# Kernel tuning notes

Hardware: AMD Instinct MI355X
Metric: run time of the kernel (lower is better)

The kernel has to match this reference:

```python
import jax, jax.numpy as jnp
import numpy as np

D_MODEL = 1024
N_HEADS = 16
D_K = D_MODEL // N_HEADS
D_FF = 4096
LN_EPS = 1e-5


def _layer_norm(x, gamma, beta):
    mu = jnp.mean(x, axis=-1, keepdims=True)
    var = jnp.mean(jnp.square(x - mu), axis=-1, keepdims=True)
    return (x - mu) * jax.lax.rsqrt(var + LN_EPS) * gamma + beta


def setup_inputs() -> dict:
    key = jax.random.key(0)
    ks = jax.random.split(key, 16)
    B, S = 2, 2048
    x = jax.random.normal(ks[0], (B, S, D_MODEL), dtype=jnp.float32)
    # causal mask: True = masked (as used by masked_fill)
    mask = ~jnp.tril(jnp.ones((S, S), dtype=bool))
    s = 1.0 / np.sqrt(D_MODEL)
    sf = 1.0 / np.sqrt(D_FF)
    inp = {
        "x": x,
        "mask": mask,
        "ln1_g": jnp.ones((D_MODEL,), jnp.float32),
        "ln1_b": jnp.zeros((D_MODEL,), jnp.float32),
        "ln2_g": jnp.ones((D_MODEL,), jnp.float32),
        "ln2_b": jnp.zeros((D_MODEL,), jnp.float32),
        "Wq": jax.random.normal(ks[1], (D_MODEL, D_MODEL), jnp.float32) * s,
        "bq": jax.random.normal(ks[2], (D_MODEL,), jnp.float32) * s,
        "Wk": jax.random.normal(ks[3], (D_MODEL, D_MODEL), jnp.float32) * s,
        "bk": jax.random.normal(ks[4], (D_MODEL,), jnp.float32) * s,
        "Wv": jax.random.normal(ks[5], (D_MODEL, D_MODEL), jnp.float32) * s,
        "bv": jax.random.normal(ks[6], (D_MODEL,), jnp.float32) * s,
        "Wo": jax.random.normal(ks[7], (D_MODEL, D_MODEL), jnp.float32) * s,
        "bo": jax.random.normal(ks[8], (D_MODEL,), jnp.float32) * s,
        "W1": jax.random.normal(ks[9], (D_MODEL, D_FF), jnp.float32) * s,
        "b1": jax.random.normal(ks[10], (D_FF,), jnp.float32) * s,
        "W2": jax.random.normal(ks[11], (D_FF, D_MODEL), jnp.float32) * sf,
        "b2": jax.random.normal(ks[12], (D_MODEL,), jnp.float32) * sf,
    }
    return inp


def reference(x, mask, ln1_g, ln1_b, ln2_g, ln2_b,
              Wq, bq, Wk, bk, Wv, bv, Wo, bo, W1, b1, W2, b2):
    B, S, _ = x.shape
    normed = _layer_norm(x, ln1_g, ln1_b)
    # project and split heads: [B, H, S, Dk]
    def split_heads(t):
        return t.reshape(B, S, N_HEADS, D_K).transpose(0, 2, 1, 3)
    Q = split_heads(normed @ Wq + bq)
    K = split_heads(normed @ Wk + bk)
    V = split_heads(normed @ Wv + bv)
    qk = jnp.einsum("bhsd,bhtd->bhst", Q, K)  # [B, H, S, S]
    qk = jnp.where(mask, -jnp.inf, qk)  # mask applied BEFORE scaling, as in source
    attn = jax.nn.softmax(qk / np.sqrt(D_K), axis=-1)
    attn_out = jnp.einsum("bhst,bhtd->bhsd", attn, V)
    attn_out = attn_out.transpose(0, 2, 1, 3).reshape(B, S, D_MODEL)
    attn_out = attn_out @ Wo + bo
    res = attn_out + x  # dropout_p=0 (eval)
    h = _layer_norm(res, ln2_g, ln2_b)
    h = jax.nn.gelu(h @ W1 + b1, approximate=False)
    h = h @ W2 + b2
    return res + h
```

## Files before the change

### kernel.cpp

```cpp
#include <hip/hip_runtime.h>


typedef __bf16 bf16;
typedef __bf16 bf16x8 __attribute__((ext_vector_type(8)));
typedef float f32x4 __attribute__((ext_vector_type(4)));

#define NROWS 4096
#define DM 1024
#define SEQ 2048
#define NHEAD 16
#define DKH 64
#define DFF 4096
#define QSCALE 0.18033688f

#define GLL16(gptr, lptr) \
  __builtin_amdgcn_global_load_lds((const __attribute__((address_space(1))) void*)(gptr), \
                                   (__attribute__((address_space(3))) void*)(lptr), 16, 0, 0)

static char* g_scratch = nullptr;
namespace {
struct ScratchInit {
  ScratchInit() {
    void* p = nullptr;
    if (hipMalloc(&p, (size_t)128 * 1024 * 1024) == hipSuccess) g_scratch = (char*)p;
  }
};
static ScratchInit g_scratch_init;
}

__global__ __launch_bounds__(256) void ln_kernel(const float* __restrict__ inp,
                                                 const float* __restrict__ gamma,
                                                 const float* __restrict__ beta,
                                                 bf16* __restrict__ out) {
  int row = blockIdx.x;
  int t = threadIdx.x;
  float4 xv = *((const float4*)(inp + (size_t)row * DM) + t);
  float v[4] = {xv.x, xv.y, xv.z, xv.w};
  float s = 0.f, sq = 0.f;
#pragma unroll
  for (int i = 0; i < 4; i++) { s += v[i]; sq += v[i] * v[i]; }
#pragma unroll
  for (int m = 32; m >= 1; m >>= 1) { s += __shfl_xor(s, m); sq += __shfl_xor(sq, m); }
  __shared__ float rs[4], rq[4];
  int w = t >> 6, lane = t & 63;
  if (lane == 0) { rs[w] = s; rq[w] = sq; }
  __syncthreads();
  s = rs[0] + rs[1] + rs[2] + rs[3];
  sq = rq[0] + rq[1] + rq[2] + rq[3];
  float mu = s * (1.f / DM);
  float var = sq * (1.f / DM) - mu * mu;
  float rinv = rsqrtf(var + 1e-5f);
  float4 gv = *((const float4*)gamma + t);
  float4 bv = *((const float4*)beta + t);
  float g[4] = {gv.x, gv.y, gv.z, gv.w}, b[4] = {bv.x, bv.y, bv.z, bv.w};
  bf16 ov[4];
#pragma unroll
  for (int i = 0; i < 4; i++) ov[i] = (bf16)((v[i] - mu) * rinv * g[i] + b[i]);
  *(uint2*)(out + (size_t)row * DM + t * 4) = *(uint2*)ov;
}

__global__ __launch_bounds__(256) void concat_bias(const float* __restrict__ bq,
                                                   const float* __restrict__ bk,
                                                   const float* __restrict__ bv,
                                                   float* __restrict__ cat) {
  int i = blockIdx.x * 256 + threadIdx.x;
  float v = (i < 1024) ? bq[i] : (i < 2048 ? bk[i - 1024] : bv[i - 2048]);
  cat[i] = v;
}

__global__ __launch_bounds__(1024) void transpose_f32_bf16(const float* __restrict__ in,
                                                           bf16* __restrict__ out,
                                                           int R, int C) {
  __shared__ bf16 tile[32][33];
  int x = blockIdx.x * 32 + threadIdx.x;
  int y = blockIdx.y * 32 + threadIdx.y;
  tile[threadIdx.y][threadIdx.x] = (bf16)in[(size_t)y * C + x];
  __syncthreads();
  int ox = blockIdx.y * 32 + threadIdx.x;
  int oy = blockIdx.x * 32 + threadIdx.y;
  out[(size_t)oy * R + ox] = tile[threadIdx.x][threadIdx.y];
}

__global__ __launch_bounds__(1024) void transpose_bf16(const bf16* __restrict__ in,
                                                       bf16* __restrict__ out,
                                                       int R, int C) {
  __shared__ bf16 tile[32][33];
  size_t zoff = (size_t)blockIdx.z * (size_t)R * (size_t)C;
  int x = blockIdx.x * 32 + threadIdx.x;
  int y = blockIdx.y * 32 + threadIdx.y;
  tile[threadIdx.y][threadIdx.x] = in[zoff + (size_t)y * C + x];
  __syncthreads();
  int ox = blockIdx.y * 32 + threadIdx.x;
  int oy = blockIdx.x * 32 + threadIdx.y;
  out[zoff + (size_t)oy * R + ox] = tile[threadIdx.x][threadIdx.y];
}

#define BM 128
#define BK 64

#define EPI_QKV3 0
#define EPI_ATTN_RES 1
#define EPI_GELU 2
#define EPI_FFN2 3

template<int EPI, int BNT>
__global__ __launch_bounds__(256, 2) void gemm_bt(
    const bf16* __restrict__ A, const bf16* __restrict__ Bt,
    const float* __restrict__ bias, int Kd, int N,
    bf16* __restrict__ outb, float* __restrict__ outf,
    const float* __restrict__ add) {
  constexpr int MS = (BNT == 128) ? 4 : 2;
  __shared__ bf16 As[BM * BK];
  __shared__ bf16 Bs[BNT * BK];
  int t = threadIdx.x;
  int m0 = blockIdx.y * BM, n0 = blockIdx.x * BNT;
  int w = t >> 6, lane = t & 63, ln = lane & 15, quad = lane >> 4;
  int wm = (BNT == 128) ? (w >> 1) * 64 : w * 32;
  int wn = (BNT == 128) ? (w & 1) * 64 : 0;
  f32x4 acc[MS][4];
#pragma unroll
  for (int i = 0; i < MS; i++)
#pragma unroll
    for (int j = 0; j < 4; j++) acc[i][j] = (f32x4){0.f, 0.f, 0.f, 0.f};

  int lr = (t >> 3) & 7, lc = t & 7;
  int gcol = ((lc ^ lr) * 8);
  const bf16* Ab = A + (size_t)(m0 + w * 8 + lr) * Kd + gcol;
  const bf16* Bb = Bt + (size_t)(n0 + w * 8 + lr) * Kd + gcol;
  bf16* AsW = As + (w * 8) * BK;
  bf16* BsW = Bs + (w * 8) * BK;

  for (int k0 = 0; k0 < Kd; k0 += BK) {
    __syncthreads();
#pragma unroll
    for (int j = 0; j < 4; j++)
      GLL16(Ab + (size_t)(32 * j) * Kd + k0, AsW + 32 * j * BK);
#pragma unroll
    for (int j = 0; j < BNT / 32; j++)
      GLL16(Bb + (size_t)(32 * j) * Kd + k0, BsW + 32 * j * BK);
    __syncthreads();
#pragma unroll
    for (int kk = 0; kk < 2; kk++) {
      bf16x8 af[MS], bfr[4];
#pragma unroll
      for (int ms = 0; ms < MS; ms++) {
        int r = wm + ms * 16 + ln;
        af[ms] = *(const bf16x8*)(As + r * BK + (((kk * 4 + quad) ^ (r & 7)) * 8));
      }
#pragma unroll
      for (int ns = 0; ns < 4; ns++) {
        int r = wn + ns * 16 + ln;
        bfr[ns] = *(const bf16x8*)(Bs + r * BK + (((kk * 4 + quad) ^ (r & 7)) * 8));
      }
#pragma unroll
      for (int ms = 0; ms < MS; ms++)
#pragma unroll
        for (int ns = 0; ns < 4; ns++)
          acc[ms][ns] = __builtin_amdgcn_mfma_f32_16x16x32_bf16(af[ms], bfr[ns], acc[ms][ns], 0, 0, 0);
    }
  }

#pragma unroll
  for (int ms = 0; ms < MS; ms++) {
#pragma unroll
    for (int ns = 0; ns < 4; ns++) {
      int col = n0 + wn + ns * 16 + ln;
      float bv = bias[col];
#pragma unroll
      for (int r = 0; r < 4; r++) {
        int row = m0 + wm + ms * 16 + quad * 4 + r;
        float val = acc[ms][ns][r] + bv;
        if (EPI == EPI_QKV3) {
          int which = col >> 10, cc = col & 1023;
          int h = cc >> 6, dk = cc & 63;
          float sc = (which == 0) ? QSCALE : 1.f;
          int b = row >> 11, sx = row & 2047;
          outb[(size_t)which * (4 << 20) +
               ((((size_t)b * NHEAD + h) * SEQ) + sx) * DKH + dk] = (bf16)(val * sc);
        } else if (EPI == EPI_ATTN_RES) {
          size_t idx = (size_t)row * DM + col;
          outf[idx] = val + add[idx];
        } else if (EPI == EPI_GELU) {
          float gl = 0.5f * val * (1.f + erff(val * 0.7071067811865475f));
          outb[(size_t)row * N + col] = (bf16)gl;
        } else {
          size_t idx = (size_t)row * DM + col;
          outf[idx] = val + add[idx];
        }
      }
    }
  }
}

#define LSTR 72
#define OSTR 68

__global__ __launch_bounds__(256) void attn_kernel(
    const bf16* __restrict__ Q, const bf16* __restrict__ K,
    const bf16* __restrict__ Vt, bf16* __restrict__ out) {
  __shared__ float smem[4608];
  int lin = blockIdx.x;
  int bh = lin & 31;
  int ii = lin >> 5;
  int t = threadIdx.x, w = t >> 6, lane = t & 63, ln = lane & 15, quad = lane >> 4;
  size_t bhS = (size_t)bh * SEQ;
  const bf16* Vg0 = Vt + (size_t)bh * DKH * SEQ;
  bf16* Pw = (bf16*)smem + w * 32 * LSTR;

  bf16x8 ones;
#pragma unroll
  for (int i = 0; i < 8; i++) ones[i] = (bf16)1.0f;

  for (int half = 0; half < 2; half++) {
    int qq = half ? ii : (63 - ii);
    int qbase = qq * 32;

    bf16x8 qa[2][2];
#pragma unroll
    for (int m = 0; m < 2; m++)
#pragma unroll
      for (int ks = 0; ks < 2; ks++)
        qa[m][ks] = *(const bf16x8*)(Q + (bhS + qbase + m * 16 + ln) * DKH + ks * 32 + quad * 8);

    f32x4 o[2][4];
#pragma unroll
    for (int m = 0; m < 2; m++)
#pragma unroll
      for (int i = 0; i < 4; i++) o[m][i] = (f32x4){0.f, 0.f, 0.f, 0.f};
    f32x4 accl[2] = {(f32x4){0.f, 0.f, 0.f, 0.f}, (f32x4){0.f, 0.f, 0.f, 0.f}};

    int ktmax = qq >> 1;
    for (int kt = w; kt <= ktmax; kt += 4) {
      const bf16* Kg = K + (bhS + kt * 64) * DKH;
      bf16x8 kbf[8], vbf[8];
#pragma unroll
      for (int ns = 0; ns < 4; ns++)
#pragma unroll
        for (int ks = 0; ks < 2; ks++)
          kbf[ns * 2 + ks] = *(const bf16x8*)(Kg + (ns * 16 + ln) * DKH + ks * 32 + quad * 8);
#pragma unroll
      for (int ns = 0; ns < 4; ns++)
#pragma unroll
        for (int ks = 0; ks < 2; ks++)
          vbf[ns * 2 + ks] = *(const bf16x8*)(Vg0 + (size_t)(ns * 16 + ln) * SEQ + kt * 64 + ks * 32 + quad * 8);

      f32x4 s[2][4];
#pragma unroll
      for (int m = 0; m < 2; m++)
#pragma unroll
        for (int ns = 0; ns < 4; ns++) s[m][ns] = (f32x4){0.f, 0.f, 0.f, 0.f};
#pragma unroll
      for (int ns = 0; ns < 4; ns++)
#pragma unroll
        for (int m = 0; m < 2; m++) {
          s[m][ns] = __builtin_amdgcn_mfma_f32_16x16x32_bf16(qa[m][0], kbf[ns * 2], s[m][ns], 0, 0, 0);
          s[m][ns] = __builtin_amdgcn_mfma_f32_16x16x32_bf16(qa[m][1], kbf[ns * 2 + 1], s[m][ns], 0, 0, 0);
        }
      if (kt == ktmax) {
#pragma unroll
        for (int m = 0; m < 2; m++)
#pragma unroll
          for (int ns = 0; ns < 4; ns++)
#pragma unroll
            for (int r = 0; r < 4; r++) {
              int qrow = qbase + m * 16 + quad * 4 + r;
              int kpos = kt * 64 + ns * 16 + ln;
              if (kpos > qrow) s[m][ns][r] = -30000.f;
            }
      }
#pragma unroll
      for (int m = 0; m < 2; m++)
#pragma unroll
        for (int ns = 0; ns < 4; ns++)
#pragma unroll
          for (int r = 0; r < 4; r++)
            Pw[(m * 16 + quad * 4 + r) * LSTR + ns * 16 + ln] =
                (bf16)__builtin_amdgcn_exp2f(s[m][ns][r]);
      bf16x8 pa[2][2];
#pragma unroll
      for (int m = 0; m < 2; m++) {
        pa[m][0] = *(const bf16x8*)(Pw + (m * 16 + ln) * LSTR + quad * 8);
        pa[m][1] = *(const bf16x8*)(Pw + (m * 16 + ln) * LSTR + 32 + quad * 8);
      }
#pragma unroll
      for (int m = 0; m < 2; m++) {
        accl[m] = __builtin_amdgcn_mfma_f32_16x16x32_bf16(pa[m][0], ones, accl[m], 0, 0, 0);
        accl[m] = __builtin_amdgcn_mfma_f32_16x16x32_bf16(pa[m][1], ones, accl[m], 0, 0, 0);
      }
#pragma unroll
      for (int ns2 = 0; ns2 < 4; ns2++)
#pragma unroll
        for (int m = 0; m < 2; m++) {
          o[m][ns2] = __builtin_amdgcn_mfma_f32_16x16x32_bf16(pa[m][0], vbf[ns2 * 2], o[m][ns2], 0, 0, 0);
          o[m][ns2] = __builtin_amdgcn_mfma_f32_16x16x32_bf16(pa[m][1], vbf[ns2 * 2 + 1], o[m][ns2], 0, 0, 0);
        }
    }

    float* Ob = smem;
    float* Lb = smem + 2 * 32 * OSTR;
    __syncthreads();
#pragma unroll
    for (int m = 0; m < 2; m++) {
      if (w < 2) {
#pragma unroll
        for (int ns2 = 0; ns2 < 4; ns2++)
#pragma unroll
          for (int r = 0; r < 4; r++)
            Ob[(w * 32 + m * 16 + quad * 4 + r) * OSTR + ns2 * 16 + ln] = o[m][ns2][r];
      }
      if (ln == 0) {
#pragma unroll
        for (int r = 0; r < 4; r++) Lb[w * 32 + m * 16 + quad * 4 + r] = accl[m][r];
      }
    }
    __syncthreads();
    if (w >= 2) {
#pragma unroll
      for (int m = 0; m < 2; m++)
#pragma unroll
        for (int ns2 = 0; ns2 < 4; ns2++)
#pragma unroll
          for (int r = 0; r < 4; r++) {
            int idx = ((w - 2) * 32 + m * 16 + quad * 4 + r) * OSTR + ns2 * 16 + ln;
            Ob[idx] += o[m][ns2][r];
          }
    }
    __syncthreads();

    int r = t >> 3, c0 = (t & 7) * 8;
    float l = Lb[r] + Lb[32 + r] + Lb[64 + r] + Lb[96 + r];
    float inv = 1.f / l;
    bf16 ov[8];
#pragma unroll
    for (int j = 0; j < 8; j++) {
      float v = Ob[r * OSTR + c0 + j] + Ob[(32 + r) * OSTR + c0 + j];
      ov[j] = (bf16)(v * inv);
    }
    int b = bh >> 4, h = bh & 15;
    *(uint4*)(out + ((size_t)b * SEQ + qbase + r) * DM + h * DKH + c0) = *(uint4*)ov;

    __syncthreads();
  }
}

extern "C" void kernel_launch(void* const* d_in, const int* in_sizes, int n_in,
                              void* d_out, int out_size, void* d_ws, size_t ws_size,
                              hipStream_t stream) {
  const float* x    = (const float*)d_in[0];
  const float* ln1g = (const float*)d_in[2];
  const float* ln1b = (const float*)d_in[3];
  const float* ln2g = (const float*)d_in[4];
  const float* ln2b = (const float*)d_in[5];
  const float* Wq = (const float*)d_in[6];   const float* bq = (const float*)d_in[7];
  const float* Wk = (const float*)d_in[8];   const float* bk = (const float*)d_in[9];
  const float* Wv = (const float*)d_in[10];  const float* bv = (const float*)d_in[11];
  const float* Wo = (const float*)d_in[12];  const float* bo = (const float*)d_in[13];
  const float* W1 = (const float*)d_in[14];  const float* b1 = (const float*)d_in[15];
  const float* W2 = (const float*)d_in[16];  const float* b2 = (const float*)d_in[17];
  float* outp = (float*)d_out;

  char* scratch = g_scratch ? g_scratch : (char*)d_ws;

  bf16* Wqt = (bf16*)scratch;
  bf16* Wkt = Wqt + (1 << 20);
  bf16* Wvt = Wkt + (1 << 20);
  bf16* Wot = Wvt + (1 << 20);
  bf16* W1t = Wot + (1 << 20);
  bf16* W2t = W1t + (4 << 20);
  bf16* normed = W2t + (4 << 20);
  bf16* Qb = normed + (4 << 20);
  bf16* Kb = Qb + (4 << 20);
  bf16* Vb = Kb + (4 << 20);
  bf16* Vtb = Vb + (4 << 20);
  bf16* attn_o = Vtb + (4 << 20);
  float* resf = (float*)(attn_o + (4 << 20));
  float* bias_cat = resf + (4 << 20);
  bf16* h1 = Qb;

  dim3 b256(256), b1k(32, 32);

  ln_kernel<<<NROWS, b256, 0, stream>>>(x, ln1g, ln1b, normed);
  concat_bias<<<12, b256, 0, stream>>>(bq, bk, bv, bias_cat);

  transpose_f32_bf16<<<dim3(32, 32), b1k, 0, stream>>>(Wq, Wqt, 1024, 1024);
  transpose_f32_bf16<<<dim3(32, 32), b1k, 0, stream>>>(Wk, Wkt, 1024, 1024);
  transpose_f32_bf16<<<dim3(32, 32), b1k, 0, stream>>>(Wv, Wvt, 1024, 1024);
  transpose_f32_bf16<<<dim3(32, 32), b1k, 0, stream>>>(Wo, Wot, 1024, 1024);
  transpose_f32_bf16<<<dim3(128, 32), b1k, 0, stream>>>(W1, W1t, 1024, 4096);
  transpose_f32_bf16<<<dim3(32, 128), b1k, 0, stream>>>(W2, W2t, 4096, 1024);

  gemm_bt<EPI_QKV3, 128><<<dim3(24, 32), b256, 0, stream>>>(
      normed, Wqt, bias_cat, 1024, 3072, Qb, nullptr, nullptr);

  transpose_bf16<<<dim3(2, 64, 32), b1k, 0, stream>>>(Vb, Vtb, 2048, 64);

  attn_kernel<<<dim3(1024), b256, 0, stream>>>(Qb, Kb, Vtb, attn_o);

  gemm_bt<EPI_ATTN_RES, 64><<<dim3(16, 32), b256, 0, stream>>>(
      attn_o, Wot, bo, 1024, 1024, nullptr, resf, x);

  ln_kernel<<<NROWS, b256, 0, stream>>>(resf, ln2g, ln2b, normed);

  gemm_bt<EPI_GELU, 128><<<dim3(32, 32), b256, 0, stream>>>(
      normed, W1t, b1, 1024, 4096, h1, nullptr, nullptr);

  gemm_bt<EPI_FFN2, 64><<<dim3(16, 32), b256, 0, stream>>>(
      h1, W2t, b2, 4096, 1024, nullptr, outp, resf);
}
```

Measured before the change: 406.8 us.

## Process 64-row query tiles per attention block to reuse K/V fragments

```diff
diff --git a/kernel.cpp b/kernel.cpp
--- a/kernel.cpp
+++ b/kernel.cpp
@@ -198,63 +198,70 @@
 __global__ __launch_bounds__(256) void attn_kernel(
     const bf16* __restrict__ Q, const bf16* __restrict__ K,
     const bf16* __restrict__ Vt, bf16* __restrict__ out) {
-  __shared__ float smem[4608];
+  __shared__ float smem[9216];
   int lin = blockIdx.x;
   int bh = lin & 31;
-  int ii = lin >> 5;
+  int jp = 31 - (lin >> 5);
   int t = threadIdx.x, w = t >> 6, lane = t & 63, ln = lane & 15, quad = lane >> 4;
+  int qbase = jp * 64;
   size_t bhS = (size_t)bh * SEQ;
   const bf16* Vg0 = Vt + (size_t)bh * DKH * SEQ;
-  bf16* Pw = (bf16*)smem + w * 32 * LSTR;
+  bf16* Pw = (bf16*)smem + w * 64 * LSTR;
+
+  bf16x8 qa[2][2][2];
+#pragma unroll
+  for (int u = 0; u < 2; u++)
+#pragma unroll
+    for (int m = 0; m < 2; m++)
+#pragma unroll
+      for (int ks = 0; ks < 2; ks++)
+        qa[u][m][ks] = *(const bf16x8*)(Q + (bhS + qbase + u * 32 + m * 16 + ln) * DKH + ks * 32 + quad * 8);
 
   bf16x8 ones;
 #pragma unroll
   for (int i = 0; i < 8; i++) ones[i] = (bf16)1.0f;
 
-  for (int half = 0; half < 2; half++) {
-    int qq = half ? ii : (63 - ii);
-    int qbase = qq * 32;
-
-    bf16x8 qa[2][2];
+  f32x4 o[2][2][4];
+#pragma unroll
+  for (int u = 0; u < 2; u++)
 #pragma unroll
     for (int m = 0; m < 2; m++)
 #pragma unroll
+      for (int i = 0; i < 4; i++) o[u][m][i] = (f32x4){0.f, 0.f, 0.f, 0.f};
+  f32x4 accl[2][2];
+#pragma unroll
+  for (int u = 0; u < 2; u++)
+#pragma unroll
+    for (int m = 0; m < 2; m++) accl[u][m] = (f32x4){0.f, 0.f, 0.f, 0.f};
+
+  int ktmax = jp;
+  for (int kt = w; kt <= ktmax; kt += 4) {
+    const bf16* Kg = K + (bhS + kt * 64) * DKH;
+    bf16x8 kbf[8], vbf[8];
+#pragma unroll
+    for (int ns = 0; ns < 4; ns++)
+#pragma unroll
       for (int ks = 0; ks < 2; ks++)
-        qa[m][ks] = *(const bf16x8*)(Q + (bhS + qbase + m * 16 + ln) * DKH + ks * 32 + quad * 8);
-
-    f32x4 o[2][4];
-#pragma unroll
-    for (int m = 0; m < 2; m++)
-#pragma unroll
-      for (int i = 0; i < 4; i++) o[m][i] = (f32x4){0.f, 0.f, 0.f, 0.f};
-    f32x4 accl[2] = {(f32x4){0.f, 0.f, 0.f, 0.f}, (f32x4){0.f, 0.f, 0.f, 0.f}};
-
-    int ktmax = qq >> 1;
-    for (int kt = w; kt <= ktmax; kt += 4) {
-      const bf16* Kg = K + (bhS + kt * 64) * DKH;
-      bf16x8 kbf[8], vbf[8];
+        kbf[ns * 2 + ks] = *(const bf16x8*)(Kg + (ns * 16 + ln) * DKH + ks * 32 + quad * 8);
+#pragma unroll
+    for (int ns = 0; ns < 4; ns++)
+#pragma unroll
+      for (int ks = 0; ks < 2; ks++)
+        vbf[ns * 2 + ks] = *(const bf16x8*)(Vg0 + (size_t)(ns * 16 + ln) * SEQ + kt * 64 + ks * 32 + quad * 8);
+
+#pragma unroll
+    for (int u = 0; u < 2; u++) {
+      f32x4 s[2][4];
+#pragma unroll
+      for (int m = 0; m < 2; m++)
+#pragma unroll
+        for (int ns = 0; ns < 4; ns++) s[m][ns] = (f32x4){0.f, 0.f, 0.f, 0.f};
 #pragma unroll
       for (int ns = 0; ns < 4; ns++)
 #pragma unroll
-        for (int ks = 0; ks < 2; ks++)
-          kbf[ns * 2 + ks] = *(const bf16x8*)(Kg + (ns * 16 + ln) * DKH + ks * 32 + quad * 8);
-#pragma unroll
-      for (int ns = 0; ns < 4; ns++)
-#pragma unroll
-        for (int ks = 0; ks < 2; ks++)
-          vbf[ns * 2 + ks] = *(const bf16x8*)(Vg0 + (size_t)(ns * 16 + ln) * SEQ + kt * 64 + ks * 32 + quad * 8);
-
-      f32x4 s[2][4];
-#pragma unroll
-      for (int m = 0; m < 2; m++)
-#pragma unroll
-        for (int ns = 0; ns < 4; ns++) s[m][ns] = (f32x4){0.f, 0.f, 0.f, 0.f};
-#pragma unroll
-      for (int ns = 0; ns < 4; ns++)
-#pragma unroll
         for (int m = 0; m < 2; m++) {
-          s[m][ns] = __builtin_amdgcn_mfma_f32_16x16x32_bf16(qa[m][0], kbf[ns * 2], s[m][ns], 0, 0, 0);
-          s[m][ns] = __builtin_amdgcn_mfma_f32_16x16x32_bf16(qa[m][1], kbf[ns * 2 + 1], s[m][ns], 0, 0, 0);
+          s[m][ns] = __builtin_amdgcn_mfma_f32_16x16x32_bf16(qa[u][m][0], kbf[ns * 2], s[m][ns], 0, 0, 0);
+          s[m][ns] = __builtin_amdgcn_mfma_f32_16x16x32_bf16(qa[u][m][1], kbf[ns * 2 + 1], s[m][ns], 0, 0, 0);
         }
       if (kt == ktmax) {
 #pragma unroll
@@ -263,7 +270,7 @@
           for (int ns = 0; ns < 4; ns++)
 #pragma unroll
             for (int r = 0; r < 4; r++) {
-              int qrow = qbase + m * 16 + quad * 4 + r;
+              int qrow = qbase + u * 32 + m * 16 + quad * 4 + r;
               int kpos = kt * 64 + ns * 16 + ln;
               if (kpos > qrow) s[m][ns][r] = -30000.f;
             }
@@ -274,31 +281,41 @@
         for (int ns = 0; ns < 4; ns++)
 #pragma unroll
           for (int r = 0; r < 4; r++)
-            Pw[(m * 16 + quad * 4 + r) * LSTR + ns * 16 + ln] =
+            Pw[(u * 32 + m * 16 + quad * 4 + r) * LSTR + ns * 16 + ln] =
                 (bf16)__builtin_amdgcn_exp2f(s[m][ns][r]);
-      bf16x8 pa[2][2];
+    }
+    bf16x8 pa[2][2][2];
+#pragma unroll
+    for (int u = 0; u < 2; u++)
 #pragma unroll
       for (int m = 0; m < 2; m++) {
-        pa[m][0] = *(const bf16x8*)(Pw + (m * 16 + ln) * LSTR + quad * 8);
-        pa[m][1] = *(const bf16x8*)(Pw + (m * 16 + ln) * LSTR + 32 + quad * 8);
-      }
+        pa[u][m][0] = *(const bf16x8*)(Pw + (u * 32 + m * 16 + ln) * LSTR + quad * 8);
+        pa[u][m][1] = *(const bf16x8*)(Pw + (u * 32 + m * 16 + ln) * LSTR + 32 + quad * 8);
+      }
+#pragma unroll
+    for (int u = 0; u < 2; u++)
 #pragma unroll
       for (int m = 0; m < 2; m++) {
-        accl[m] = __builtin_amdgcn_mfma_f32_16x16x32_bf16(pa[m][0], ones, accl[m], 0, 0, 0);
-        accl[m] = __builtin_amdgcn_mfma_f32_16x16x32_bf16(pa[m][1], ones, accl[m], 0, 0, 0);
-      }
-#pragma unroll
-      for (int ns2 = 0; ns2 < 4; ns2++)
+        accl[u][m] = __builtin_amdgcn_mfma_f32_16x16x32_bf16(pa[u][m][0], ones, accl[u][m], 0, 0, 0);
+        accl[u][m] = __builtin_amdgcn_mfma_f32_16x16x32_bf16(pa[u][m][1], ones, accl[u][m], 0, 0, 0);
+      }
+#pragma unroll
+    for (int ns2 = 0; ns2 < 4; ns2++)
+#pragma unroll
+      for (int u = 0; u < 2; u++)
 #pragma unroll
         for (int m = 0; m < 2; m++) {
-          o[m][ns2] = __builtin_amdgcn_mfma_f32_16x16x32_bf16(pa[m][0], vbf[ns2 * 2], o[m][ns2], 0, 0, 0);
-          o[m][ns2] = __builtin_amdgcn_mfma_f32_16x16x32_bf16(pa[m][1], vbf[ns2 * 2 + 1], o[m][ns2], 0, 0, 0);
+          o[u][m][ns2] = __builtin_amdgcn_mfma_f32_16x16x32_bf16(pa[u][m][0], vbf[ns2 * 2], o[u][m][ns2], 0, 0, 0);
+          o[u][m][ns2] = __builtin_amdgcn_mfma_f32_16x16x32_bf16(pa[u][m][1], vbf[ns2 * 2 + 1], o[u][m][ns2], 0, 0, 0);
         }
-    }
-
-    float* Ob = smem;
-    float* Lb = smem + 2 * 32 * OSTR;
-    __syncthreads();
+  }
+
+  constexpr int SLAB = 64 * OSTR;
+  float* Ob = smem;
+  float* Lb = smem + 2 * SLAB;
+  __syncthreads();
+#pragma unroll
+  for (int u = 0; u < 2; u++)
 #pragma unroll
     for (int m = 0; m < 2; m++) {
       if (w < 2) {
@@ -306,40 +323,43 @@
         for (int ns2 = 0; ns2 < 4; ns2++)
 #pragma unroll
           for (int r = 0; r < 4; r++)
-            Ob[(w * 32 + m * 16 + quad * 4 + r) * OSTR + ns2 * 16 + ln] = o[m][ns2][r];
+            Ob[w * SLAB + (u * 32 + m * 16 + quad * 4 + r) * OSTR + ns2 * 16 + ln] = o[u][m][ns2][r];
       }
       if (ln == 0) {
 #pragma unroll
-        for (int r = 0; r < 4; r++) Lb[w * 32 + m * 16 + quad * 4 + r] = accl[m][r];
+        for (int r = 0; r < 4; r++) Lb[w * 64 + u * 32 + m * 16 + quad * 4 + r] = accl[u][m][r];
       }
     }
-    __syncthreads();
-    if (w >= 2) {
+  __syncthreads();
+  if (w >= 2) {
+#pragma unroll
+    for (int u = 0; u < 2; u++)
 #pragma unroll
       for (int m = 0; m < 2; m++)
 #pragma unroll
         for (int ns2 = 0; ns2 < 4; ns2++)
 #pragma unroll
           for (int r = 0; r < 4; r++) {
-            int idx = ((w - 2) * 32 + m * 16 + quad * 4 + r) * OSTR + ns2 * 16 + ln;
-            Ob[idx] += o[m][ns2][r];
+            int idx = (w - 2) * SLAB + (u * 32 + m * 16 + quad * 4 + r) * OSTR + ns2 * 16 + ln;
+            Ob[idx] += o[u][m][ns2][r];
           }
-    }
-    __syncthreads();
-
-    int r = t >> 3, c0 = (t & 7) * 8;
-    float l = Lb[r] + Lb[32 + r] + Lb[64 + r] + Lb[96 + r];
+  }
+  __syncthreads();
+
+  int r32 = t >> 3, c0 = (t & 7) * 8;
+  int b = bh >> 4, h = bh & 15;
+#pragma unroll
+  for (int u = 0; u < 2; u++) {
+    int row = u * 32 + r32;
+    float l = Lb[row] + Lb[64 + row] + Lb[128 + row] + Lb[192 + row];
     float inv = 1.f / l;
     bf16 ov[8];
 #pragma unroll
     for (int j = 0; j < 8; j++) {
-      float v = Ob[r * OSTR + c0 + j] + Ob[(32 + r) * OSTR + c0 + j];
+      float v = Ob[row * OSTR + c0 + j] + Ob[SLAB + row * OSTR + c0 + j];
       ov[j] = (bf16)(v * inv);
     }
-    int b = bh >> 4, h = bh & 15;
-    *(uint4*)(out + ((size_t)b * SEQ + qbase + r) * DM + h * DKH + c0) = *(uint4*)ov;
-
-    __syncthreads();
+    *(uint4*)(out + ((size_t)b * SEQ + qbase + row) * DM + h * DKH + c0) = *(uint4*)ov;
   }
 }
 
```

Result: faster. 398.3 us (-2.1%).
